# Optimization experiments

Hardware: AMD Instinct MI355X
Metric: run time of the kernel (lower is better)

## Reference

```python
import jax, jax.numpy as jnp
import numpy as np
from jax import lax

I, H, O, L = 8, 50, 6, 3
B, T = 4096, 256


def setup_inputs() -> dict:
    key = jax.random.key(0)
    ks = jax.random.split(key, 16)
    s = 1.0 / np.sqrt(H)  # PyTorch LSTM init scale
    inp = {"x": jax.random.normal(ks[0], (B, T, I), dtype=jnp.float32)}
    in_dims = [I, H, H]
    ki = 1
    for l in range(L):
        inp[f"w_ih{l}"] = jax.random.uniform(ks[ki], (4 * H, in_dims[l]), minval=-s, maxval=s); ki += 1
        inp[f"w_hh{l}"] = jax.random.uniform(ks[ki], (4 * H, H), minval=-s, maxval=s); ki += 1
        inp[f"b_ih{l}"] = jax.random.uniform(ks[ki], (4 * H,), minval=-s, maxval=s); ki += 1
        inp[f"b_hh{l}"] = jax.random.uniform(ks[ki], (4 * H,), minval=-s, maxval=s); ki += 1
    inp["w_fc"] = jax.random.uniform(ks[13], (O, H), minval=-s, maxval=s)
    inp["b_fc"] = jax.random.uniform(ks[14], (O,), minval=-s, maxval=s)
    return inp


def _lstm_layer(x, w_ih, w_hh, b_ih, b_hh):
    # x: [B, T, in]; returns [B, T, H]. PyTorch gate order: i, f, g, o.
    b = b_ih + b_hh
    pre = jnp.einsum('bti,gi->btg', x, w_ih) + b  # input projections for all steps at once
    h0 = jnp.zeros((x.shape[0], H), x.dtype)
    c0 = jnp.zeros((x.shape[0], H), x.dtype)

    def step(carry, p_t):
        h, c = carry
        gates = p_t + h @ w_hh.T
        i, f, g, o = jnp.split(gates, 4, axis=-1)
        i = jax.nn.sigmoid(i); f = jax.nn.sigmoid(f)
        g = jnp.tanh(g); o = jax.nn.sigmoid(o)
        c = f * c + i * g
        h = o * jnp.tanh(c)
        return (h, c), h

    (_, _), hs = lax.scan(step, (h0, c0), jnp.swapaxes(pre, 0, 1))  # [T, B, H]
    return jnp.swapaxes(hs, 0, 1)


def reference(x, w_ih0, w_hh0, b_ih0, b_hh0, w_ih1, w_hh1, b_ih1, b_hh1,
              w_ih2, w_hh2, b_ih2, b_hh2, w_fc, b_fc):
    h = _lstm_layer(x, w_ih0, w_hh0, b_ih0, b_hh0)
    h = _lstm_layer(h, w_ih1, w_hh1, b_ih1, b_hh1)
    h = _lstm_layer(h, w_ih2, w_hh2, b_ih2, b_hh2)
    last = h[:, -1, :]  # [B, H]
    return last @ w_fc.T + b_fc  # [B, O]
```

## Files before the change

kernel.cpp:

```cpp
#include <hip/hip_runtime.h>
#include <hip/hip_bf16.h>
#include <cstddef>


#define T_STEPS 256
#define NGRP    43
#define BTOT    4096
#define NTHR    768
#define GS      128
#define BUFR    1152

typedef __attribute__((ext_vector_type(8))) _Float16 half8;
typedef __attribute__((ext_vector_type(4))) float    f32x4;

#define BAR() do { \
    asm volatile("s_waitcnt lgkmcnt(0)" ::: "memory"); \
    __builtin_amdgcn_sched_barrier(0); \
    __builtin_amdgcn_s_barrier(); \
    __builtin_amdgcn_sched_barrier(0); \
} while (0)

__device__ __forceinline__ unsigned short f2h(float x) {
    union { _Float16 h; unsigned short s; } u;
    u.h = (_Float16)x;
    return u.s;
}

__device__ __forceinline__ float cell_upd(f32x4 g, float& cst) {
    const float K2 = 2.8853900817779268f;
    float eg  = __builtin_amdgcn_exp2f(fminf(fmaxf(g[2], -126.0f), 126.0f));
    float ei  = __builtin_amdgcn_exp2f(g[0]);
    float ef  = __builtin_amdgcn_exp2f(g[1]);
    float eo  = __builtin_amdgcn_exp2f(g[3]);
    float itg = (eg - 1.0f) * __builtin_amdgcn_rcpf((1.0f + ei) * (1.0f + eg));
    float fg  = __builtin_amdgcn_rcpf(1.0f + ef);
    float c   = fmaf(fg, cst, itg);
    cst = c;
    float ec  = __builtin_amdgcn_exp2f(fminf(fmaxf(K2 * c, -126.0f), 126.0f));
    return (ec - 1.0f) * __builtin_amdgcn_rcpf((1.0f + eo) * (1.0f + ec));
}

template<bool L0M, int NT, int KS>
__device__ __forceinline__ void load_wb(int T0, int lane,
    const float* __restrict__ w_ih, const float* __restrict__ w_hh,
    const float* __restrict__ b_ih, const float* __restrict__ b_hh,
    half8 (&W)[NT][KS])
{
    const float K1 = 1.4426950408889634f, K2 = 2.8853900817779268f;
    const int m = lane & 15, kg = lane >> 4;
    #pragma unroll
    for (int q = 0; q < NT; ++q) {
        int gp = (T0 + q) * 16 + m;
        int gr = (gp < 200) ? ((gp & 3) * 50 + (gp >> 2)) : -1;
        float scale = ((gp & 3) == 2) ? K2 : -K1;
        #pragma unroll
        for (int ks = 0; ks < KS; ++ks)
            #pragma unroll
            for (int e = 0; e < 8; ++e) {
                int k = ks * 32 + kg * 8 + e;
                float v = 0.0f;
                if (gr >= 0) {
                    if (L0M) {
                        if (k < 8) v = w_ih[gr * 8 + k];
                        else if (k < 58) v = w_hh[gr * 50 + (k - 8)];
                        else if (k == 58) v = b_ih[gr] + b_hh[gr];
                    } else {
                        if (k < 50) v = w_ih[gr * 50 + k];
                        else if (k == 50) v = b_ih[gr] + b_hh[gr];
                        else if (k >= 64 && k < 114) v = w_hh[gr * 50 + (k - 64)];
                    }
                }
                W[q][ks][e] = (_Float16)(v * scale);
            }
    }
}

template<int T0, int NT, bool XST>
__device__ void role_l0(int lane, int b0, const float* __restrict__ xf,
    const float* w_ih, const float* w_hh, const float* b_ih, const float* b_hh,
    short (*H0)[BUFR])
{
    half8 W[NT][2];
    load_wb<true, NT, 2>(T0, lane, w_ih, w_hh, b_ih, b_hh, W);
    float cst[NT];
    #pragma unroll
    for (int q = 0; q < NT; ++q) cst[q] = 0.0f;
    const int b = lane & 15, kg = lane >> 4;
    const int o0 = kg * GS + b * 8;
    const int o4 = (4 + kg) * GS + b * 8;
    int wof[NT];
    #pragma unroll
    for (int q = 0; q < NT; ++q) {
        int n = (T0 + q) * 4 + kg;
        wof[q] = (1 + (n >> 3)) * GS + b * 8 + (n & 7);
    }

    for (int ii = 0; ii < NGRP; ++ii) {
        #pragma unroll
        for (int p = 0; p < 6; ++p) {
            const int it = ii * 6 + p;
            const bool stg = XST && (kg == 0) && (it + 1 < T_STEPS);
            float4 xa, xb2;
            if (stg) {
                const float* xr = &xf[((size_t)(b0 + b) * T_STEPS + (it + 1)) * 8];
                xa  = *(const float4*)xr;
                xb2 = *(const float4*)(xr + 4);
            }
            if (it < T_STEPS) {
                const short* rb = H0[p & 1];
                short*       wb = H0[(p + 1) & 1];
                half8 A0 = *(const half8*)&rb[o0];
                half8 A1 = *(const half8*)&rb[o4];
                f32x4 accA[NT], accB[NT];
                #pragma unroll
                for (int q = 0; q < NT; ++q) {
                    accA[q] = (f32x4){0.0f, 0.0f, 0.0f, 0.0f};
                    accB[q] = (f32x4){0.0f, 0.0f, 0.0f, 0.0f};
                }
                #pragma unroll
                for (int q = 0; q < NT; ++q)
                    accA[q] = __builtin_amdgcn_mfma_f32_16x16x32_f16(W[q][0], A0, accA[q], 0, 0, 0);
                #pragma unroll
                for (int q = 0; q < NT; ++q)
                    accB[q] = __builtin_amdgcn_mfma_f32_16x16x32_f16(W[q][1], A1, accB[q], 0, 0, 0);
                #pragma unroll
                for (int q = 0; q < NT; ++q) {
                    int n = (T0 + q) * 4 + kg;
                    if (n < 50) {
                        float h = cell_upd(accA[q] + accB[q], cst[q]);
                        wb[wof[q]] = (short)f2h(h);
                    }
                }
            }
            if (stg) {
                short hi[8];
                hi[0] = (short)f2h(xa.x);  hi[1] = (short)f2h(xa.y);
                hi[2] = (short)f2h(xa.z);  hi[3] = (short)f2h(xa.w);
                hi[4] = (short)f2h(xb2.x); hi[5] = (short)f2h(xb2.y);
                hi[6] = (short)f2h(xb2.z); hi[7] = (short)f2h(xb2.w);
                *(half8*)&H0[(p + 1) & 1][b * 8] = *(half8*)hi;
            }
            BAR();
        }
    }
}

template<int T0, bool LASTL>
__device__ void role_mid(int lane,
    const float* w_ih, const float* w_hh, const float* b_ih, const float* b_hh,
    short (*H0)[BUFR], short (*H1)[BUFR], short (*H2)[BUFR], float* hfp)
{
    constexpr int SKEW = LASTL ? 2 : 1;
    half8 W[3][4];
    load_wb<false, 3, 4>(T0, lane, w_ih, w_hh, b_ih, b_hh, W);
    float cst[3] = {0.0f, 0.0f, 0.0f};
    const int b = lane & 15, kg = lane >> 4;
    const int o1 = (1 + kg) * GS + b * 8;
    const int o5 = (5 + kg) * GS + b * 8;
    int wof[3];
    #pragma unroll
    for (int q = 0; q < 3; ++q) {
        int n = (T0 + q) * 4 + kg;
        wof[q] = (1 + (n >> 3)) * GS + b * 8 + (n & 7);
    }

    for (int ii = 0; ii < NGRP; ++ii) {
        #pragma unroll
        for (int p = 0; p < 6; ++p) {
            const int it = ii * 6 + p;
            const int t = it - SKEW;
            if ((unsigned)t < T_STEPS) {
                const short* xsb = LASTL ? H1[(p + 1) % 3] : H0[p & 1];
                const short* hsb = LASTL ? H2[(p + 1) & 1] : H1[(p + 1) % 3];
                short*       wb  = LASTL ? H2[p & 1]       : H1[(p + 2) % 3];

                half8 Ap0 = *(const half8*)&xsb[o1];
                half8 Ap1 = *(const half8*)&xsb[o5];
                half8 Ap2 = *(const half8*)&hsb[o1];
                half8 Ap3 = *(const half8*)&hsb[o5];

                f32x4 accA[3], accB[3];
                #pragma unroll
                for (int q = 0; q < 3; ++q) {
                    accA[q] = (f32x4){0.0f, 0.0f, 0.0f, 0.0f};
                    accB[q] = (f32x4){0.0f, 0.0f, 0.0f, 0.0f};
                }
                #pragma unroll
                for (int q = 0; q < 3; ++q)
                    accA[q] = __builtin_amdgcn_mfma_f32_16x16x32_f16(W[q][0], Ap0, accA[q], 0, 0, 0);
                #pragma unroll
                for (int q = 0; q < 3; ++q)
                    accB[q] = __builtin_amdgcn_mfma_f32_16x16x32_f16(W[q][1], Ap1, accB[q], 0, 0, 0);
                #pragma unroll
                for (int q = 0; q < 3; ++q)
                    accA[q] = __builtin_amdgcn_mfma_f32_16x16x32_f16(W[q][2], Ap2, accA[q], 0, 0, 0);
                #pragma unroll
                for (int q = 0; q < 3; ++q)
                    accB[q] = __builtin_amdgcn_mfma_f32_16x16x32_f16(W[q][3], Ap3, accB[q], 0, 0, 0);

                #pragma unroll
                for (int q = 0; q < 3; ++q) {
                    int n = (T0 + q) * 4 + kg;
                    if (n < 50) {
                        float h = cell_upd(accA[q] + accB[q], cst[q]);
                        wb[wof[q]] = (short)f2h(h);
                        if (LASTL && t == T_STEPS - 1) hfp[b * 56 + n] = h;
                    }
                }
            }
            BAR();
        }
    }
}

__device__ void role_orphan(int lane,
    const float* w_ih1, const float* w_hh1, const float* b_ih1, const float* b_hh1,
    const float* w_ih2, const float* w_hh2, const float* b_ih2, const float* b_hh2,
    short (*H0)[BUFR], short (*H1)[BUFR], short (*H2)[BUFR], float* hfp)
{
    half8 W1[1][4], W2[1][4];
    load_wb<false, 1, 4>(12, lane, w_ih1, w_hh1, b_ih1, b_hh1, W1);
    load_wb<false, 1, 4>(12, lane, w_ih2, w_hh2, b_ih2, b_hh2, W2);
    float c1 = 0.0f, c2 = 0.0f;
    const int b = lane & 15, kg = lane >> 4;
    const int o1 = (1 + kg) * GS + b * 8;
    const int o5 = (5 + kg) * GS + b * 8;
    const int n  = 48 + kg;
    const int wof = (1 + (n >> 3)) * GS + b * 8 + (n & 7);

    for (int ii = 0; ii < NGRP; ++ii) {
        #pragma unroll
        for (int p = 0; p < 6; ++p) {
            const int it = ii * 6 + p;
            const int t1 = it - 1, t2 = it - 2;
            const bool d1 = (unsigned)t1 < T_STEPS, d2 = (unsigned)t2 < T_STEPS;

            half8 A1[4], A2[4];
            if (d1) {
                const short* xsb = H0[p & 1];
                const short* hsb = H1[(p + 1) % 3];
                A1[0] = *(const half8*)&xsb[o1];
                A1[1] = *(const half8*)&xsb[o5];
                A1[2] = *(const half8*)&hsb[o1];
                A1[3] = *(const half8*)&hsb[o5];
            }
            if (d2) {
                const short* xsb = H1[(p + 1) % 3];
                const short* hsb = H2[(p + 1) & 1];
                A2[0] = *(const half8*)&xsb[o1];
                A2[1] = *(const half8*)&xsb[o5];
                A2[2] = *(const half8*)&hsb[o1];
                A2[3] = *(const half8*)&hsb[o5];
            }

            f32x4 a1 = (f32x4){0.0f, 0.0f, 0.0f, 0.0f};
            f32x4 a2 = (f32x4){0.0f, 0.0f, 0.0f, 0.0f};
            #pragma unroll
            for (int ks = 0; ks < 4; ++ks) {
                if (d1) a1 = __builtin_amdgcn_mfma_f32_16x16x32_f16(W1[0][ks], A1[ks], a1, 0, 0, 0);
                if (d2) a2 = __builtin_amdgcn_mfma_f32_16x16x32_f16(W2[0][ks], A2[ks], a2, 0, 0, 0);
            }

            if (d1 && kg < 2) {
                float h = cell_upd(a1, c1);
                H1[(p + 2) % 3][wof] = (short)f2h(h);
            }
            if (d2 && kg < 2) {
                float h = cell_upd(a2, c2);
                H2[p & 1][wof] = (short)f2h(h);
                if (t2 == T_STEPS - 1) hfp[b * 56 + n] = h;
            }
            BAR();
        }
    }
}

__global__ __launch_bounds__(NTHR) void lstm_fused(
    const float* __restrict__ xf,
    const float* w_ih0, const float* w_hh0, const float* b_ih0, const float* b_hh0,
    const float* w_ih1, const float* w_hh1, const float* b_ih1, const float* b_hh1,
    const float* w_ih2, const float* w_hh2, const float* b_ih2, const float* b_hh2,
    const float* __restrict__ w_fc, const float* __restrict__ b_fc,
    float* __restrict__ out)
{
    __shared__ __align__(16) short H0[2][BUFR];
    __shared__ __align__(16) short H1[3][BUFR];
    __shared__ __align__(16) short H2[2][BUFR];
    __shared__ __align__(16) float hf[16 * 56];

    const int tid  = threadIdx.x;
    const int lane = tid & 63;
    const int wid  = tid >> 6;
    const int b0   = blockIdx.x * 16;

    for (int i = tid; i < 2 * BUFR; i += NTHR) { ((short*)H0)[i] = 0; ((short*)H2)[i] = 0; }
    for (int i = tid; i < 3 * BUFR; i += NTHR) ((short*)H1)[i] = 0;
    __syncthreads();

    if (tid < 80) {
        int bufi = tid >> 4, b = tid & 15;
        short* bp = (bufi < 2) ? H0[bufi] : H1[bufi - 2];
        bp[7 * GS + b * 8 + 2] = (short)0x3C00;
    }
    if (tid < 16) {
        int b = tid;
        #pragma unroll
        for (int j = 0; j < 8; ++j) {
            float v = xf[((size_t)(b0 + b) * T_STEPS + 0) * 8 + j];
            H0[0][b * 8 + j] = (short)f2h(v);
        }
    }
    __syncthreads();

    if      (wid == 0)  role_l0<0, 5, false>(lane, b0, xf, w_ih0, w_hh0, b_ih0, b_hh0, H0);
    else if (wid == 1)  role_l0<5, 4, false>(lane, b0, xf, w_ih0, w_hh0, b_ih0, b_hh0, H0);
    else if (wid == 2)  role_l0<9, 4, true >(lane, b0, xf, w_ih0, w_hh0, b_ih0, b_hh0, H0);
    else if (wid == 3)  role_mid<0, false>(lane, w_ih1, w_hh1, b_ih1, b_hh1, H0, H1, H2, nullptr);
    else if (wid == 4)  role_mid<3, false>(lane, w_ih1, w_hh1, b_ih1, b_hh1, H0, H1, H2, nullptr);
    else if (wid == 5)  role_mid<6, false>(lane, w_ih1, w_hh1, b_ih1, b_hh1, H0, H1, H2, nullptr);
    else if (wid == 6)  role_mid<9, false>(lane, w_ih1, w_hh1, b_ih1, b_hh1, H0, H1, H2, nullptr);
    else if (wid == 7)  role_mid<0, true >(lane, w_ih2, w_hh2, b_ih2, b_hh2, H0, H1, H2, hf);
    else if (wid == 8)  role_mid<3, true >(lane, w_ih2, w_hh2, b_ih2, b_hh2, H0, H1, H2, hf);
    else if (wid == 9)  role_mid<6, true >(lane, w_ih2, w_hh2, b_ih2, b_hh2, H0, H1, H2, hf);
    else if (wid == 10) role_mid<9, true >(lane, w_ih2, w_hh2, b_ih2, b_hh2, H0, H1, H2, hf);
    else                role_orphan(lane,
                            w_ih1, w_hh1, b_ih1, b_hh1,
                            w_ih2, w_hh2, b_ih2, b_hh2,
                            H0, H1, H2, hf);

    __syncthreads();

    if (tid < 96) {
        int b = tid / 6, o = tid - b * 6;
        float a = b_fc[o];
        #pragma unroll
        for (int u = 0; u < 50; ++u)
            a = fmaf(w_fc[o * 50 + u], hf[b * 56 + u], a);
        out[(size_t)(b0 + b) * 6 + o] = a;
    }
}

extern "C" void kernel_launch(void* const* d_in, const int* in_sizes, int n_in,
                              void* d_out, int out_size, void* d_ws, size_t ws_size,
                              hipStream_t stream) {
    (void)in_sizes; (void)n_in; (void)d_ws; (void)ws_size; (void)out_size;

    const float* x     = (const float*)d_in[0];
    const float* w_ih0 = (const float*)d_in[1];
    const float* w_hh0 = (const float*)d_in[2];
    const float* b_ih0 = (const float*)d_in[3];
    const float* b_hh0 = (const float*)d_in[4];
    const float* w_ih1 = (const float*)d_in[5];
    const float* w_hh1 = (const float*)d_in[6];
    const float* b_ih1 = (const float*)d_in[7];
    const float* b_hh1 = (const float*)d_in[8];
    const float* w_ih2 = (const float*)d_in[9];
    const float* w_hh2 = (const float*)d_in[10];
    const float* b_ih2 = (const float*)d_in[11];
    const float* b_hh2 = (const float*)d_in[12];
    const float* w_fc  = (const float*)d_in[13];
    const float* b_fc  = (const float*)d_in[14];
    float* out = (float*)d_out;

    lstm_fused<<<dim3(BTOT / 16), dim3(NTHR), 0, stream>>>(
        x, w_ih0, w_hh0, b_ih0, b_hh0, w_ih1, w_hh1, b_ih1, b_hh1,
        w_ih2, w_hh2, b_ih2, b_hh2, w_fc, b_fc, out);
}
```

Baseline: 247.0 us.

## Spread LSTM gate tiles over 16 waves and drop the orphan role

Raises the block from 12 to 16 waves and redistributes the 13 gate tiles per layer. Layer 0 now uses 4 waves and layers 1 and 2 use 6 waves each, with 2-3 tiles per wave instead of 3-5. The combined orphan wave that handled the final tile of both layers 1 and 2 is removed. The aim is to shorten the critical path per timestep between barriers, at the cost of more waves joining every barrier and a bigger block that may lower occupancy.

Measured after the change: 248.4 us. Within noise of the previous version (+0.6%).

```diff
diff --git a/kernel.cpp b/kernel.cpp
--- a/kernel.cpp
+++ b/kernel.cpp
@@ -6,7 +6,7 @@
 #define T_STEPS 256
 #define NGRP    43
 #define BTOT    4096
-#define NTHR    768
+#define NTHR    1024
 #define GS      128
 #define BUFR    1152
 
@@ -145,21 +145,23 @@
     }
 }
 
-template<int T0, bool LASTL>
+template<int T0, int NT, bool LASTL>
 __device__ void role_mid(int lane,
     const float* w_ih, const float* w_hh, const float* b_ih, const float* b_hh,
     short (*H0)[BUFR], short (*H1)[BUFR], short (*H2)[BUFR], float* hfp)
 {
     constexpr int SKEW = LASTL ? 2 : 1;
-    half8 W[3][4];
-    load_wb<false, 3, 4>(T0, lane, w_ih, w_hh, b_ih, b_hh, W);
-    float cst[3] = {0.0f, 0.0f, 0.0f};
+    half8 W[NT][4];
+    load_wb<false, NT, 4>(T0, lane, w_ih, w_hh, b_ih, b_hh, W);
+    float cst[NT];
+    #pragma unroll
+    for (int q = 0; q < NT; ++q) cst[q] = 0.0f;
     const int b = lane & 15, kg = lane >> 4;
     const int o1 = (1 + kg) * GS + b * 8;
     const int o5 = (5 + kg) * GS + b * 8;
-    int wof[3];
-    #pragma unroll
-    for (int q = 0; q < 3; ++q) {
+    int wof[NT];
+    #pragma unroll
+    for (int q = 0; q < NT; ++q) {
         int n = (T0 + q) * 4 + kg;
         wof[q] = (1 + (n >> 3)) * GS + b * 8 + (n & 7);
     }
@@ -179,27 +181,27 @@
                 half8 Ap2 = *(const half8*)&hsb[o1];
                 half8 Ap3 = *(const half8*)&hsb[o5];
 
-                f32x4 accA[3], accB[3];
-                #pragma unroll
-                for (int q = 0; q < 3; ++q) {
+                f32x4 accA[NT], accB[NT];
+                #pragma unroll
+                for (int q = 0; q < NT; ++q) {
                     accA[q] = (f32x4){0.0f, 0.0f, 0.0f, 0.0f};
                     accB[q] = (f32x4){0.0f, 0.0f, 0.0f, 0.0f};
                 }
                 #pragma unroll
-                for (int q = 0; q < 3; ++q)
+                for (int q = 0; q < NT; ++q)
                     accA[q] = __builtin_amdgcn_mfma_f32_16x16x32_f16(W[q][0], Ap0, accA[q], 0, 0, 0);
                 #pragma unroll
-                for (int q = 0; q < 3; ++q)
+                for (int q = 0; q < NT; ++q)
                     accB[q] = __builtin_amdgcn_mfma_f32_16x16x32_f16(W[q][1], Ap1, accB[q], 0, 0, 0);
                 #pragma unroll
-                for (int q = 0; q < 3; ++q)
+                for (int q = 0; q < NT; ++q)
                     accA[q] = __builtin_amdgcn_mfma_f32_16x16x32_f16(W[q][2], Ap2, accA[q], 0, 0, 0);
                 #pragma unroll
-                for (int q = 0; q < 3; ++q)
+                for (int q = 0; q < NT; ++q)
                     accB[q] = __builtin_amdgcn_mfma_f32_16x16x32_f16(W[q][3], Ap3, accB[q], 0, 0, 0);
 
                 #pragma unroll
-                for (int q = 0; q < 3; ++q) {
+                for (int q = 0; q < NT; ++q) {
                     int n = (T0 + q) * 4 + kg;
                     if (n < 50) {
                         float h = cell_upd(accA[q] + accB[q], cst[q]);
@@ -207,68 +209,6 @@
                         if (LASTL && t == T_STEPS - 1) hfp[b * 56 + n] = h;
                     }
                 }
-            }
-            BAR();
-        }
-    }
-}
-
-__device__ void role_orphan(int lane,
-    const float* w_ih1, const float* w_hh1, const float* b_ih1, const float* b_hh1,
-    const float* w_ih2, const float* w_hh2, const float* b_ih2, const float* b_hh2,
-    short (*H0)[BUFR], short (*H1)[BUFR], short (*H2)[BUFR], float* hfp)
-{
-    half8 W1[1][4], W2[1][4];
-    load_wb<false, 1, 4>(12, lane, w_ih1, w_hh1, b_ih1, b_hh1, W1);
-    load_wb<false, 1, 4>(12, lane, w_ih2, w_hh2, b_ih2, b_hh2, W2);
-    float c1 = 0.0f, c2 = 0.0f;
-    const int b = lane & 15, kg = lane >> 4;
-    const int o1 = (1 + kg) * GS + b * 8;
-    const int o5 = (5 + kg) * GS + b * 8;
-    const int n  = 48 + kg;
-    const int wof = (1 + (n >> 3)) * GS + b * 8 + (n & 7);
-
-    for (int ii = 0; ii < NGRP; ++ii) {
-        #pragma unroll
-        for (int p = 0; p < 6; ++p) {
-            const int it = ii * 6 + p;
-            const int t1 = it - 1, t2 = it - 2;
-            const bool d1 = (unsigned)t1 < T_STEPS, d2 = (unsigned)t2 < T_STEPS;
-
-            half8 A1[4], A2[4];
-            if (d1) {
-                const short* xsb = H0[p & 1];
-                const short* hsb = H1[(p + 1) % 3];
-                A1[0] = *(const half8*)&xsb[o1];
-                A1[1] = *(const half8*)&xsb[o5];
-                A1[2] = *(const half8*)&hsb[o1];
-                A1[3] = *(const half8*)&hsb[o5];
-            }
-            if (d2) {
-                const short* xsb = H1[(p + 1) % 3];
-                const short* hsb = H2[(p + 1) & 1];
-                A2[0] = *(const half8*)&xsb[o1];
-                A2[1] = *(const half8*)&xsb[o5];
-                A2[2] = *(const half8*)&hsb[o1];
-                A2[3] = *(const half8*)&hsb[o5];
-            }
-
-            f32x4 a1 = (f32x4){0.0f, 0.0f, 0.0f, 0.0f};
-            f32x4 a2 = (f32x4){0.0f, 0.0f, 0.0f, 0.0f};
-            #pragma unroll
-            for (int ks = 0; ks < 4; ++ks) {
-                if (d1) a1 = __builtin_amdgcn_mfma_f32_16x16x32_f16(W1[0][ks], A1[ks], a1, 0, 0, 0);
-                if (d2) a2 = __builtin_amdgcn_mfma_f32_16x16x32_f16(W2[0][ks], A2[ks], a2, 0, 0, 0);
-            }
-
-            if (d1 && kg < 2) {
-                float h = cell_upd(a1, c1);
-                H1[(p + 2) % 3][wof] = (short)f2h(h);
-            }
-            if (d2 && kg < 2) {
-                float h = cell_upd(a2, c2);
-                H2[p & 1][wof] = (short)f2h(h);
-                if (t2 == T_STEPS - 1) hfp[b * 56 + n] = h;
             }
             BAR();
         }
@@ -312,21 +252,22 @@
     }
     __syncthreads();
 
-    if      (wid == 0)  role_l0<0, 5, false>(lane, b0, xf, w_ih0, w_hh0, b_ih0, b_hh0, H0);
-    else if (wid == 1)  role_l0<5, 4, false>(lane, b0, xf, w_ih0, w_hh0, b_ih0, b_hh0, H0);
-    else if (wid == 2)  role_l0<9, 4, true >(lane, b0, xf, w_ih0, w_hh0, b_ih0, b_hh0, H0);
-    else if (wid == 3)  role_mid<0, false>(lane, w_ih1, w_hh1, b_ih1, b_hh1, H0, H1, H2, nullptr);
-    else if (wid == 4)  role_mid<3, false>(lane, w_ih1, w_hh1, b_ih1, b_hh1, H0, H1, H2, nullptr);
-    else if (wid == 5)  role_mid<6, false>(lane, w_ih1, w_hh1, b_ih1, b_hh1, H0, H1, H2, nullptr);
-    else if (wid == 6)  role_mid<9, false>(lane, w_ih1, w_hh1, b_ih1, b_hh1, H0, H1, H2, nullptr);
-    else if (wid == 7)  role_mid<0, true >(lane, w_ih2, w_hh2, b_ih2, b_hh2, H0, H1, H2, hf);
-    else if (wid == 8)  role_mid<3, true >(lane, w_ih2, w_hh2, b_ih2, b_hh2, H0, H1, H2, hf);
-    else if (wid == 9)  role_mid<6, true >(lane, w_ih2, w_hh2, b_ih2, b_hh2, H0, H1, H2, hf);
-    else if (wid == 10) role_mid<9, true >(lane, w_ih2, w_hh2, b_ih2, b_hh2, H0, H1, H2, hf);
-    else                role_orphan(lane,
-                            w_ih1, w_hh1, b_ih1, b_hh1,
-                            w_ih2, w_hh2, b_ih2, b_hh2,
-                            H0, H1, H2, hf);
+    if      (wid == 0)  role_l0<0,  4, false>(lane, b0, xf, w_ih0, w_hh0, b_ih0, b_hh0, H0);
+    else if (wid == 1)  role_l0<4,  3, false>(lane, b0, xf, w_ih0, w_hh0, b_ih0, b_hh0, H0);
+    else if (wid == 2)  role_l0<7,  3, false>(lane, b0, xf, w_ih0, w_hh0, b_ih0, b_hh0, H0);
+    else if (wid == 3)  role_l0<10, 3, true >(lane, b0, xf, w_ih0, w_hh0, b_ih0, b_hh0, H0);
+    else if (wid == 4)  role_mid<0,  3, false>(lane, w_ih1, w_hh1, b_ih1, b_hh1, H0, H1, H2, nullptr);
+    else if (wid == 5)  role_mid<3,  2, false>(lane, w_ih1, w_hh1, b_ih1, b_hh1, H0, H1, H2, nullptr);
+    else if (wid == 6)  role_mid<5,  2, false>(lane, w_ih1, w_hh1, b_ih1, b_hh1, H0, H1, H2, nullptr);
+    else if (wid == 7)  role_mid<7,  2, false>(lane, w_ih1, w_hh1, b_ih1, b_hh1, H0, H1, H2, nullptr);
+    else if (wid == 8)  role_mid<9,  2, false>(lane, w_ih1, w_hh1, b_ih1, b_hh1, H0, H1, H2, nullptr);
+    else if (wid == 9)  role_mid<11, 2, false>(lane, w_ih1, w_hh1, b_ih1, b_hh1, H0, H1, H2, nullptr);
+    else if (wid == 10) role_mid<0,  3, true >(lane, w_ih2, w_hh2, b_ih2, b_hh2, H0, H1, H2, hf);
+    else if (wid == 11) role_mid<3,  2, true >(lane, w_ih2, w_hh2, b_ih2, b_hh2, H0, H1, H2, hf);
+    else if (wid == 12) role_mid<5,  2, true >(lane, w_ih2, w_hh2, b_ih2, b_hh2, H0, H1, H2, hf);
+    else if (wid == 13) role_mid<7,  2, true >(lane, w_ih2, w_hh2, b_ih2, b_hh2, H0, H1, H2, hf);
+    else if (wid == 14) role_mid<9,  2, true >(lane, w_ih2, w_hh2, b_ih2, b_hh2, H0, H1, H2, hf);
+    else                role_mid<11, 2, true >(lane, w_ih2, w_hh2, b_ih2, b_hh2, H0, H1, H2, hf);
 
     __syncthreads();
 
```
